# Kernel tuning notes

Hardware: AMD Instinct MI355X
Metric: run time of the kernel (lower is better)

The kernel has to match this reference:

```python
import jax, jax.numpy as jnp
import numpy as np

NUM_GRAPHS = 1024
NODES_PER_GRAPH = 128
AVG_DEG = 16
NODE_FEATS = 128
K = 20
TOTAL_LATENT = 97  # sum(latent_dim) = 32+32+32+1


def _init_params(key):
    def lin(k, fi, fo):
        s = 1.0 / np.sqrt(fi)
        kw, kb = jax.random.split(k)
        return (jax.random.uniform(kw, (fi, fo), jnp.float32, -s, s),
                jax.random.uniform(kb, (fo,), jnp.float32, -s, s))
    ks = jax.random.split(key, 9)
    p = {}
    p['W1'], p['b1'] = lin(ks[0], NODE_FEATS + 1, 32)
    p['W2'], p['b2'] = lin(ks[1], 32, 32)
    p['W3'], p['b3'] = lin(ks[2], 32, 32)
    p['W4'], p['b4'] = lin(ks[3], 32, 1)
    s = 1.0 / np.sqrt(TOTAL_LATENT)
    p['c1_w'] = jax.random.uniform(ks[4], (16, TOTAL_LATENT), jnp.float32, -s, s)
    p['c1_b'] = jnp.zeros((16,), jnp.float32)
    s2 = 1.0 / np.sqrt(16 * 5)
    p['c2_w'] = jax.random.uniform(ks[5], (32, 16, 5), jnp.float32, -s2, s2)
    p['c2_b'] = jnp.zeros((32,), jnp.float32)
    p['out_w'], p['out_b'] = lin(ks[6], 192, 1024)
    p['h1_w'], p['h1_b'] = lin(ks[7], 1024, 128)
    p['h2_w'], p['h2_b'] = lin(ks[8], 128, 16)
    return p


def setup_inputs() -> dict:
    key = jax.random.key(0)
    k_x, k_e, k_p = jax.random.split(key, 3)
    G, P, D = NUM_GRAPHS, NODES_PER_GRAPH, AVG_DEG
    N, E = G * P, G * P * D
    rng = np.random.default_rng(0)
    gid = np.repeat(np.arange(G, dtype=np.int64), P * D)
    src = gid * P + rng.integers(0, P, size=E)
    dst = gid * P + rng.integers(0, P, size=E)
    order = np.argsort(src, kind='stable')  # rows sorted by source node (matches slicing assumption)
    edge_index = jnp.asarray(np.stack([src[order], dst[order]]), dtype=jnp.int32)
    inp = {'x': jax.random.normal(k_x, (N, NODE_FEATS), jnp.float32),
           'edge_attr': jax.random.uniform(k_e, (E, 1), jnp.float32),
           'edge_index': edge_index}
    inp.update(_init_params(k_p))
    return inp


def reference(x, edge_attr, edge_index, W1, b1, W2, b2, W3, b3, W4, b4,
              c1_w, c1_b, c2_w, c2_b, out_w, out_b, h1_w, h1_b, h2_w, h2_b):
    N = x.shape[0]
    row, col = edge_index[0], edge_index[1]
    # per-source-node sum of incident edge attrs (replaces the Python slicing loop)
    x_edge = jax.ops.segment_sum(edge_attr, row, num_segments=N)  # [N,1]
    h = jnp.concatenate([x, x_edge], axis=1)  # [N, F+1]
    # GCN symmetric normalization with self-loops (PyG GCNConv default)
    deg = 1.0 + jax.ops.segment_sum(jnp.ones_like(col, dtype=jnp.float32), col, num_segments=N)
    dis = jax.lax.rsqrt(deg)
    enorm = dis[row] * dis[col]      # per-edge norm
    self_norm = dis * dis            # self-loop norm

    def gcn(h, W, b):
        h = h @ W
        agg = jax.ops.segment_sum(h[row] * enorm[:, None], col, num_segments=N)
        return agg + h * self_norm[:, None] + b

    o1 = gcn(h, W1, b1)
    o2 = gcn(o1, W2, b2)
    o3 = gcn(o2, W3, b3)
    o4 = gcn(o3, W4, b4)  # [N,1]
    feat = jnp.concatenate([o1, o2, o3, o4], axis=1)  # [N, 97]

    G = NUM_GRAPHS
    P = N // G
    scores = o4.reshape(G, P)
    _, idx = jax.lax.top_k(scores, K)  # per-graph top-k node indices (descending, sorted)
    pooled = jnp.take_along_axis(feat.reshape(G, P, TOTAL_LATENT), idx[:, :, None], axis=1)  # [G,K,97]

    # Conv1d(1,16,kernel=97,stride=97) over flattened [G,1,K*97] == per-slot matmul
    c1 = jax.nn.relu(jnp.einsum('gkd,cd->gck', pooled, c1_w) + c1_b[None, :, None])  # [G,16,K]
    mp = c1.reshape(G, 16, K // 2, 2).max(axis=-1)  # MaxPool1d(2,2) -> [G,16,10]
    c2 = jax.lax.conv_general_dilated(mp, c2_w, (1,), 'VALID',
                                      dimension_numbers=('NCH', 'OIH', 'NCH'))
    c2 = jax.nn.relu(c2 + c2_b[None, :, None])  # [G,32,6]
    dense = c2.reshape(G, -1)  # [G,192]
    d1 = jax.nn.relu(dense @ out_w + out_b)
    d2 = jax.nn.relu(d1 @ h1_w + h1_b)  # dropout is identity in eval mode
    logits = d2 @ h2_w + h2_b
    return jax.nn.log_softmax(logits, axis=1)
```

## Files before the change

### kernel.cpp

```cpp
#include <hip/hip_runtime.h>

typedef __attribute__((ext_vector_type(4))) float f4;
typedef __attribute__((ext_vector_type(2))) float f2;

#define NP 128
#define NE 2048
#define NFEAT 128
#define LW 33
#define NT 512

__device__ __forceinline__ void aggregate(float* zo, const float* __restrict__ bias,
    const unsigned char* inlist, const int* offs4, const int* indeg,
    const float* diss, int t)
{
  const int c = t >> 2;
  const int j0 = (t & 3) * 8;
  float s[8];
#pragma unroll
  for (int u = 0; u < 8; ++u) s[u] = zo[c*LW + j0 + u];
  const int ps = offs4[c];
  const int pe = ps + ((indeg[c] + 3) & ~3);
  for (int p = ps; p < pe; p += 4) {
    const unsigned w = *(const unsigned*)(inlist + p);
#pragma unroll
    for (int b = 0; b < 4; ++b) {
      const int rr = (w >> (8*b)) & 255;
#pragma unroll
      for (int u = 0; u < 8; ++u) s[u] += zo[rr*LW + j0 + u];
    }
  }
  __syncthreads();
  const float d = diss[c];
#pragma unroll
  for (int u = 0; u < 8; ++u) zo[c*LW + j0 + u] = d * s[u] + bias[j0 + u];
  __syncthreads();
}

__device__ __forceinline__ void mm32(const float* src, float* dst,
    const float* __restrict__ Wg, float* Wl, const float* diss, int t)
{
  if (t < 256) {
    const int k = t >> 3, jq = t & 7;
    *(f4*)&Wl[k*36 + jq*4] = *(const f4*)(Wg + (size_t)k*32 + jq*4);
  }
  __syncthreads();
  const int n2 = t & 63, c4 = t >> 6;
  float acc[2][4];
#pragma unroll
  for (int i = 0; i < 2; ++i)
#pragma unroll
    for (int u = 0; u < 4; ++u) acc[i][u] = 0.f;
#pragma unroll
  for (int k = 0; k < 32; ++k) {
    f4 w = *(const f4*)&Wl[k*36 + c4*4];
    const float a0 = src[n2*LW + k];
    const float a1 = src[(n2+64)*LW + k];
#pragma unroll
    for (int u = 0; u < 4; ++u) { acc[0][u] += a0 * w[u]; acc[1][u] += a1 * w[u]; }
  }
#pragma unroll
  for (int i = 0; i < 2; ++i) {
    const int n = n2 + 64*i;
    const float dd = diss[n];
#pragma unroll
    for (int u = 0; u < 4; ++u) dst[n*LW + c4*4 + u] = acc[i][u] * dd;
  }
}

__global__ __launch_bounds__(NT, 4) void k1_gcn(
    const float* __restrict__ x, const float* __restrict__ eattr,
    const int* __restrict__ eidx,
    const float* __restrict__ W1, const float* __restrict__ b1,
    const float* __restrict__ W2, const float* __restrict__ b2,
    const float* __restrict__ W3, const float* __restrict__ b3,
    const float* __restrict__ W4, const float* __restrict__ b4,
    const float* __restrict__ c1w, const float* __restrict__ c1b,
    const float* __restrict__ c2w, const float* __restrict__ c2b,
    float* __restrict__ dense_out, int E_total)
{
  __shared__ float o1[129*LW];
  __shared__ float o2[129*LW];
  __shared__ float o3[129*LW];
  __shared__ float Wl[32*36];
  __shared__ float o4s[129];
  __shared__ float xedge[NP];
  __shared__ float diss[NP];
  __shared__ int indeg[NP];
  __shared__ int offs4[NP];
  __shared__ int curp[NP];
  __shared__ unsigned char inlist[2432];

  const int t = threadIdx.x;
  const int g = blockIdx.x;
  const int ebase = g * NE;
  const int nbase = g * NP;

  if (t < NP) { xedge[t] = 0.f; indeg[t] = 0; curp[t] = 0; }
  for (int w = t; w < 608; w += NT) ((int*)inlist)[w] = (int)0x80808080u;
  __syncthreads();

  int er[4], ec[4];
#pragma unroll
  for (int i = 0; i < 4; ++i) {
    const int e = t + i * NT;
    er[i] = eidx[ebase + e] - nbase;
    ec[i] = eidx[E_total + ebase + e] - nbase;
    atomicAdd(&xedge[er[i]], eattr[ebase + e]);
    atomicAdd(&indeg[ec[i]], 1);
  }
  __syncthreads();

  if (t < NP) {
    int s = 0;
    for (int m = 0; m < NP; ++m) { const int dd = (indeg[m] + 3) & ~3; s += (m < t) ? dd : 0; }
    offs4[t] = s;
    diss[t] = rsqrtf(1.0f + (float)indeg[t]);
  }
  __syncthreads();

#pragma unroll
  for (int i = 0; i < 4; ++i) {
    const int p = atomicAdd(&curp[ec[i]], 1);
    inlist[offs4[ec[i]] + p] = (unsigned char)er[i];
  }

  {
    float* xs = o2;
    const int n2 = t & 63, c4 = t >> 6;
    const int sn = t >> 2, sq = t & 3;
    const float* xrow = x + (size_t)(nbase + sn) * NFEAT + sq * 8;
    f4 pv0 = *(const f4*)(xrow);
    f4 pv1 = *(const f4*)(xrow + 4);
    float acc[2][4];
#pragma unroll
    for (int i = 0; i < 2; ++i)
#pragma unroll
      for (int u = 0; u < 4; ++u) acc[i][u] = 0.f;

    for (int fc = 0; fc < NFEAT; fc += 32) {
      __syncthreads();
      {
        float* xd = xs + sn * LW + sq * 8;
#pragma unroll
        for (int j = 0; j < 4; ++j) xd[j] = pv0[j];
#pragma unroll
        for (int j = 0; j < 4; ++j) xd[4 + j] = pv1[j];
      }
      if (t < 256) {
        const int k = t >> 3, jq = t & 7;
        *(f4*)&Wl[k*36 + jq*4] = *(const f4*)(W1 + (size_t)(fc + k) * 32 + jq * 4);
      }
      if (fc < 96) {
        pv0 = *(const f4*)(xrow + fc + 32);
        pv1 = *(const f4*)(xrow + fc + 36);
      }
      __syncthreads();
#pragma unroll
      for (int k = 0; k < 32; ++k) {
        f4 w = *(const f4*)&Wl[k*36 + c4*4];
        const float a0 = xs[n2*LW + k];
        const float a1 = xs[(n2+64)*LW + k];
#pragma unroll
        for (int u = 0; u < 4; ++u) { acc[0][u] += a0 * w[u]; acc[1][u] += a1 * w[u]; }
      }
    }
    f4 wlast = *(const f4*)(W1 + 128*32 + c4*4);
#pragma unroll
    for (int i = 0; i < 2; ++i) {
      const int n = n2 + 64*i;
      const float xe = xedge[n], dd = diss[n];
#pragma unroll
      for (int u = 0; u < 4; ++u)
        o1[n*LW + c4*4 + u] = (acc[i][u] + xe * wlast[u]) * dd;
    }
  }
  __syncthreads();
  if (t < LW) { o1[128*LW + t] = 0.f; o2[128*LW + t] = 0.f; o3[128*LW + t] = 0.f; }
  if (t == 0) o4s[128] = 0.f;
  __syncthreads();

  aggregate(o1, b1, inlist, offs4, indeg, diss, t);
  mm32(o1, o2, W2, Wl, diss, t);
  __syncthreads();
  aggregate(o2, b2, inlist, offs4, indeg, diss, t);
  mm32(o2, o3, W3, Wl, diss, t);
  __syncthreads();
  aggregate(o3, b3, inlist, offs4, indeg, diss, t);

  if (t < NP) {
    float s = 0.f;
#pragma unroll
    for (int f = 0; f < 32; ++f) s += o3[t*LW + f] * W4[f];
    o4s[t] = s * diss[t];
  }
  __syncthreads();
  float s4 = 0.f;
  if (t < NP) {
    s4 = o4s[t];
    const int ps = offs4[t], pe = ps + ((indeg[t] + 3) & ~3);
    for (int p = ps; p < pe; p += 4) {
      const unsigned w = *(const unsigned*)(inlist + p);
#pragma unroll
      for (int b = 0; b < 4; ++b) s4 += o4s[(w >> (8*b)) & 255];
    }
  }
  __syncthreads();
  if (t < NP) o4s[t] = diss[t] * s4 + b4[0];
  __syncthreads();

  int* selidx   = (int*)Wl;
  float* c1buf  = Wl + 32;
  float* mpbuf  = Wl + 352;
  if (t < NP) {
    const float sn = o4s[t];
    int cnt = 0;
    for (int m = 0; m < NP; ++m) {
      const float sm = o4s[m];
      cnt += (sm > sn || (sm == sn && m < t)) ? 1 : 0;
    }
    if (cnt < 20) selidx[cnt] = t;
  }
  __syncthreads();

  if (t < 320) {
    const int k = t % 20, ch = t / 20;
    const int nd = selidx[k];
    const float* wr = c1w + ch * 97;
    float s = c1b[ch];
#pragma unroll 8
    for (int d = 0; d < 32; ++d) s += o1[nd*LW + d] * wr[d];
#pragma unroll 8
    for (int d = 0; d < 32; ++d) s += o2[nd*LW + d] * wr[32 + d];
#pragma unroll 8
    for (int d = 0; d < 32; ++d) s += o3[nd*LW + d] * wr[64 + d];
    s += o4s[nd] * wr[96];
    c1buf[ch*20 + k] = fmaxf(s, 0.f);
  }
  __syncthreads();
  if (t < 160) {
    const int ch = t / 10, p = t % 10;
    mpbuf[ch*10 + p] = fmaxf(c1buf[ch*20 + 2*p], c1buf[ch*20 + 2*p + 1]);
  }
  __syncthreads();
  if (t < 192) {
    const int oc = t / 6, tt = t % 6;
    float s = c2b[oc];
#pragma unroll
    for (int ic = 0; ic < 16; ++ic) {
      const float* wr = c2w + (oc * 16 + ic) * 5;
#pragma unroll
      for (int u = 0; u < 5; ++u) s += mpbuf[ic*10 + tt + u] * wr[u];
    }
    dense_out[(size_t)g * 192 + t] = fmaxf(s, 0.f);
  }
}

__global__ __launch_bounds__(256) void k2_d1(const float* __restrict__ dense,
    const float* __restrict__ out_w, const float* __restrict__ out_b,
    float* __restrict__ d1)
{
  __shared__ float As[32 * 68];
  __shared__ float Bs[32 * 68];
  const int t = threadIdx.x;
  const int n0 = blockIdx.x * 64, m0 = blockIdx.y * 64;
  const int r = t & 15, c = t >> 4;
  float acc[4][4];
#pragma unroll
  for (int i = 0; i < 4; ++i)
#pragma unroll
    for (int u = 0; u < 4; ++u) acc[i][u] = 0.f;

  for (int kk = 0; kk < 192; kk += 32) {
    __syncthreads();
    {
      const int m = t >> 2;
      const int kq = (t & 3) * 2;
#pragma unroll
      for (int q = 0; q < 2; ++q) {
        f4 v = *(const f4*)(dense + (size_t)(m0 + m) * 192 + kk + (kq + q) * 4);
        const int k0 = (kq + q) * 4;
        As[(k0+0)*68 + m] = v[0]; As[(k0+1)*68 + m] = v[1];
        As[(k0+2)*68 + m] = v[2]; As[(k0+3)*68 + m] = v[3];
      }
    }
    {
      const int k = t >> 3;
      const int nq = (t & 7) * 2;
#pragma unroll
      for (int q = 0; q < 2; ++q) {
        f4 v = *(const f4*)(out_w + (size_t)(kk + k) * 1024 + n0 + (nq + q) * 4);
        *(f4*)&Bs[k*68 + (nq + q) * 4] = v;
      }
    }
    __syncthreads();
#pragma unroll
    for (int k = 0; k < 32; ++k) {
      f4 a = *(const f4*)&As[k*68 + r*4];
      f4 b = *(const f4*)&Bs[k*68 + c*4];
#pragma unroll
      for (int i = 0; i < 4; ++i)
#pragma unroll
        for (int u = 0; u < 4; ++u) acc[i][u] += a[i] * b[u];
    }
  }
  f4 bb = *(const f4*)(out_b + n0 + c*4);
#pragma unroll
  for (int i = 0; i < 4; ++i) {
    f4 o;
#pragma unroll
    for (int u = 0; u < 4; ++u) o[u] = fmaxf(acc[i][u] + bb[u], 0.f);
    *(f4*)(d1 + (size_t)(m0 + r*4 + i) * 1024 + n0 + c*4) = o;
  }
}

__global__ __launch_bounds__(256) void k3_init(const float* __restrict__ h1_b,
    float* __restrict__ d2)
{
  const int i = blockIdx.x * 256 + threadIdx.x;
  d2[i] = h1_b[i & 127];
}

__global__ __launch_bounds__(256) void k3_d2(const float* __restrict__ d1,
    const float* __restrict__ h1_w, float* __restrict__ d2)
{
  __shared__ float As[32 * 36];
  __shared__ float Bs[32 * 36];
  const int t = threadIdx.x;
  const int m0 = blockIdx.x * 32, n0 = blockIdx.y * 32, ks = blockIdx.z * 128;
  const int r = t & 15, c = t >> 4;
  float a00 = 0.f, a01 = 0.f, a10 = 0.f, a11 = 0.f;

  for (int kk = ks; kk < ks + 128; kk += 32) {
    __syncthreads();
    {
      const int m = t >> 3, kq = t & 7;
      f4 v = *(const f4*)(d1 + (size_t)(m0 + m) * 1024 + kk + kq * 4);
      const int k0 = kq * 4;
      As[(k0+0)*36 + m] = v[0]; As[(k0+1)*36 + m] = v[1];
      As[(k0+2)*36 + m] = v[2]; As[(k0+3)*36 + m] = v[3];
    }
    {
      const int k = t >> 3, nq = t & 7;
      f4 v = *(const f4*)(h1_w + (size_t)(kk + k) * 128 + n0 + nq * 4);
      *(f4*)&Bs[k*36 + nq*4] = v;
    }
    __syncthreads();
#pragma unroll
    for (int k = 0; k < 32; ++k) {
      f2 a = *(const f2*)&As[k*36 + r*2];
      f2 b = *(const f2*)&Bs[k*36 + c*2];
      a00 += a[0]*b[0]; a01 += a[0]*b[1];
      a10 += a[1]*b[0]; a11 += a[1]*b[1];
    }
  }
  atomicAdd(d2 + (size_t)(m0 + r*2 + 0) * 128 + n0 + c*2 + 0, a00);
  atomicAdd(d2 + (size_t)(m0 + r*2 + 0) * 128 + n0 + c*2 + 1, a01);
  atomicAdd(d2 + (size_t)(m0 + r*2 + 1) * 128 + n0 + c*2 + 0, a10);
  atomicAdd(d2 + (size_t)(m0 + r*2 + 1) * 128 + n0 + c*2 + 1, a11);
}

__global__ __launch_bounds__(256) void k4_out(const float* __restrict__ d2,
    const float* __restrict__ h2_w, const float* __restrict__ h2_b,
    float* __restrict__ outp)
{
  __shared__ float lbuf[16][17];
  const int t = threadIdx.x;
  const int gl = t >> 4, cc = t & 15;
  const int g = blockIdx.x * 16 + gl;
  float s = h2_b[cc];
  for (int k4 = 0; k4 < 32; ++k4) {
    f4 v = *(const f4*)(d2 + (size_t)g * 128 + k4 * 4);
#pragma unroll
    for (int i = 0; i < 4; ++i) {
      const float rv = fmaxf(v[i], 0.f);
      s += rv * h2_w[(k4*4 + i) * 16 + cc];
    }
  }
  lbuf[gl][cc] = s;
  __syncthreads();
  float mx = -1e30f;
#pragma unroll
  for (int j = 0; j < 16; ++j) mx = fmaxf(mx, lbuf[gl][j]);
  float se = 0.f;
#pragma unroll
  for (int j = 0; j < 16; ++j) se += expf(lbuf[gl][j] - mx);
  outp[(size_t)g * 16 + cc] = s - mx - logf(se);
}

extern "C" void kernel_launch(void* const* d_in, const int* in_sizes, int n_in,
                              void* d_out, int out_size, void* d_ws, size_t ws_size,
                              hipStream_t stream) {
  const float* x     = (const float*)d_in[0];
  const float* eattr = (const float*)d_in[1];
  const int*   eidx  = (const int*)d_in[2];
  const float* W1 = (const float*)d_in[3];  const float* b1 = (const float*)d_in[4];
  const float* W2 = (const float*)d_in[5];  const float* b2 = (const float*)d_in[6];
  const float* W3 = (const float*)d_in[7];  const float* b3 = (const float*)d_in[8];
  const float* W4 = (const float*)d_in[9];  const float* b4 = (const float*)d_in[10];
  const float* c1w = (const float*)d_in[11]; const float* c1b = (const float*)d_in[12];
  const float* c2w = (const float*)d_in[13]; const float* c2b = (const float*)d_in[14];
  const float* out_w = (const float*)d_in[15]; const float* out_b = (const float*)d_in[16];
  const float* h1_w  = (const float*)d_in[17]; const float* h1_b  = (const float*)d_in[18];
  const float* h2_w  = (const float*)d_in[19]; const float* h2_b  = (const float*)d_in[20];

  const int E_total = in_sizes[1];
  const int N_nodes = in_sizes[0] / NFEAT;
  const int G = N_nodes / NP;

  float* ws    = (float*)d_ws;
  float* dense = ws;
  float* d1    = ws + (size_t)G * 192;
  float* d2    = d1 + (size_t)G * 1024;

  k1_gcn<<<G, NT, 0, stream>>>(x, eattr, eidx, W1, b1, W2, b2, W3, b3, W4, b4,
                               c1w, c1b, c2w, c2b, dense, E_total);
  k2_d1<<<dim3(16, G / 64), 256, 0, stream>>>(dense, out_w, out_b, d1);
  k3_init<<<(G * 128) / 256, 256, 0, stream>>>(h1_b, d2);
  k3_d2<<<dim3(G / 32, 4, 8), 256, 0, stream>>>(d1, h1_w, d2);
  k4_out<<<G / 16, 256, 0, stream>>>(d2, h2_w, h2_b, (float*)d_out);
}
```

Measured before the change: 141.9 us.

## Pad rows to 36 floats, vectorize aggregation, read weights from global

Changes the per-node LDS row stride from 33 to 36 so that aggregation and matmuls can use float4 loads and stores. Aggregation now walks an unpadded byte adjacency list one neighbor at a time instead of in padded groups of four, which removes the sentinel row and the list initialization. The matmuls are remapped so each wavefront owns an 8-column slice of 64 nodes and reads weights from global memory with wave-uniform addresses, dropping the LDS weight staging and its barrier. The first-layer input is double-buffered across o2/o3, and the k3 inner loop switches from float2 to scalar LDS reads. The risk is more LDS bank conflicts with the stride-36 layout and extra global/scalar weight traffic.

```diff
diff --git a/kernel.cpp b/kernel.cpp
--- a/kernel.cpp
+++ b/kernel.cpp
@@ -1,70 +1,60 @@
 #include <hip/hip_runtime.h>
 
 typedef __attribute__((ext_vector_type(4))) float f4;
-typedef __attribute__((ext_vector_type(2))) float f2;
 
 #define NP 128
 #define NE 2048
 #define NFEAT 128
-#define LW 33
+#define LW 36
 #define NT 512
 
 __device__ __forceinline__ void aggregate(float* zo, const float* __restrict__ bias,
-    const unsigned char* inlist, const int* offs4, const int* indeg,
+    const unsigned char* inlist, const int* offs, const int* indeg,
     const float* diss, int t)
 {
   const int c = t >> 2;
   const int j0 = (t & 3) * 8;
-  float s[8];
-#pragma unroll
-  for (int u = 0; u < 8; ++u) s[u] = zo[c*LW + j0 + u];
-  const int ps = offs4[c];
-  const int pe = ps + ((indeg[c] + 3) & ~3);
-  for (int p = ps; p < pe; p += 4) {
-    const unsigned w = *(const unsigned*)(inlist + p);
-#pragma unroll
-    for (int b = 0; b < 4; ++b) {
-      const int rr = (w >> (8*b)) & 255;
-#pragma unroll
-      for (int u = 0; u < 8; ++u) s[u] += zo[rr*LW + j0 + u];
-    }
+  float* zr = zo + c * LW + j0;
+  f4 s0 = *(const f4*)zr;
+  f4 s1 = *(const f4*)(zr + 4);
+  const int ps = offs[c], pe = ps + indeg[c];
+  for (int p = ps; p < pe; ++p) {
+    const int rr = inlist[p];
+    const float* nr = zo + rr * LW + j0;
+    s0 += *(const f4*)nr;
+    s1 += *(const f4*)(nr + 4);
   }
   __syncthreads();
   const float d = diss[c];
-#pragma unroll
-  for (int u = 0; u < 8; ++u) zo[c*LW + j0 + u] = d * s[u] + bias[j0 + u];
+  const f4 b0 = *(const f4*)(bias + j0);
+  const f4 b1 = *(const f4*)(bias + j0 + 4);
+  *(f4*)zr = s0 * d + b0;
+  *(f4*)(zr + 4) = s1 * d + b1;
   __syncthreads();
 }
 
 __device__ __forceinline__ void mm32(const float* src, float* dst,
-    const float* __restrict__ Wg, float* Wl, const float* diss, int t)
-{
-  if (t < 256) {
-    const int k = t >> 3, jq = t & 7;
-    *(f4*)&Wl[k*36 + jq*4] = *(const f4*)(Wg + (size_t)k*32 + jq*4);
-  }
-  __syncthreads();
-  const int n2 = t & 63, c4 = t >> 6;
-  float acc[2][4];
-#pragma unroll
-  for (int i = 0; i < 2; ++i)
-#pragma unroll
-    for (int u = 0; u < 4; ++u) acc[i][u] = 0.f;
+    const float* __restrict__ Wg, const float* diss, int t)
+{
+  const int wv = __builtin_amdgcn_readfirstlane(t >> 6);
+  const int j0 = (wv & 3) * 8;
+  const int c  = ((wv >> 2) * 64) + (t & 63);
+  f4 av[8];
+#pragma unroll
+  for (int j = 0; j < 8; ++j) av[j] = *(const f4*)(src + c * LW + 4 * j);
+  f4 a0 = {0.f, 0.f, 0.f, 0.f}, a1 = {0.f, 0.f, 0.f, 0.f};
 #pragma unroll
   for (int k = 0; k < 32; ++k) {
-    f4 w = *(const f4*)&Wl[k*36 + c4*4];
-    const float a0 = src[n2*LW + k];
-    const float a1 = src[(n2+64)*LW + k];
-#pragma unroll
-    for (int u = 0; u < 4; ++u) { acc[0][u] += a0 * w[u]; acc[1][u] += a1 * w[u]; }
-  }
-#pragma unroll
-  for (int i = 0; i < 2; ++i) {
-    const int n = n2 + 64*i;
-    const float dd = diss[n];
-#pragma unroll
-    for (int u = 0; u < 4; ++u) dst[n*LW + c4*4 + u] = acc[i][u] * dd;
-  }
+    const float a = av[k >> 2][k & 3];
+    const float* wr = Wg + k * 32 + j0;
+    const f4 w0 = *(const f4*)wr;
+    const f4 w1 = *(const f4*)(wr + 4);
+    a0 += a * w0;
+    a1 += a * w1;
+  }
+  const float d = diss[c];
+  *(f4*)(dst + c * LW + j0) = a0 * d;
+  *(f4*)(dst + c * LW + j0 + 4) = a1 * d;
 }
 
 __global__ __launch_bounds__(NT, 4) void k1_gcn(
@@ -78,17 +68,19 @@
     const float* __restrict__ c2w, const float* __restrict__ c2b,
     float* __restrict__ dense_out, int E_total)
 {
-  __shared__ float o1[129*LW];
-  __shared__ float o2[129*LW];
-  __shared__ float o3[129*LW];
-  __shared__ float Wl[32*36];
-  __shared__ float o4s[129];
+  __shared__ float o1[NP * LW];
+  __shared__ float o2[NP * LW];
+  __shared__ float o3[NP * LW];
+  __shared__ float o4s[NP];
   __shared__ float xedge[NP];
   __shared__ float diss[NP];
   __shared__ int indeg[NP];
-  __shared__ int offs4[NP];
+  __shared__ int offs[NP];
   __shared__ int curp[NP];
-  __shared__ unsigned char inlist[2432];
+  __shared__ unsigned char inlist[NE];
+  __shared__ int selidx[20];
+  __shared__ float c1buf[16 * 20];
+  __shared__ float mpbuf[16 * 10];
 
   const int t = threadIdx.x;
   const int g = blockIdx.x;
@@ -96,7 +88,6 @@
   const int nbase = g * NP;
 
   if (t < NP) { xedge[t] = 0.f; indeg[t] = 0; curp[t] = 0; }
-  for (int w = t; w < 608; w += NT) ((int*)inlist)[w] = (int)0x80808080u;
   __syncthreads();
 
   int er[4], ec[4];
@@ -112,8 +103,8 @@
 
   if (t < NP) {
     int s = 0;
-    for (int m = 0; m < NP; ++m) { const int dd = (indeg[m] + 3) & ~3; s += (m < t) ? dd : 0; }
-    offs4[t] = s;
+    for (int m = 0; m < NP; ++m) s += (m < t) ? indeg[m] : 0;
+    offs[t] = s;
     diss[t] = rsqrtf(1.0f + (float)indeg[t]);
   }
   __syncthreads();
@@ -121,96 +112,77 @@
 #pragma unroll
   for (int i = 0; i < 4; ++i) {
     const int p = atomicAdd(&curp[ec[i]], 1);
-    inlist[offs4[ec[i]] + p] = (unsigned char)er[i];
+    inlist[offs[ec[i]] + p] = (unsigned char)er[i];
   }
 
   {
-    float* xs = o2;
-    const int n2 = t & 63, c4 = t >> 6;
+    const int wv = __builtin_amdgcn_readfirstlane(t >> 6);
+    const int j0 = (wv & 3) * 8;
+    const int c  = ((wv >> 2) * 64) + (t & 63);
     const int sn = t >> 2, sq = t & 3;
     const float* xrow = x + (size_t)(nbase + sn) * NFEAT + sq * 8;
     f4 pv0 = *(const f4*)(xrow);
     f4 pv1 = *(const f4*)(xrow + 4);
-    float acc[2][4];
-#pragma unroll
-    for (int i = 0; i < 2; ++i)
-#pragma unroll
-      for (int u = 0; u < 4; ++u) acc[i][u] = 0.f;
+    f4 a0 = {0.f, 0.f, 0.f, 0.f}, a1 = {0.f, 0.f, 0.f, 0.f};
 
     for (int fc = 0; fc < NFEAT; fc += 32) {
+      float* xs = (fc & 32) ? o3 : o2;
       __syncthreads();
-      {
-        float* xd = xs + sn * LW + sq * 8;
-#pragma unroll
-        for (int j = 0; j < 4; ++j) xd[j] = pv0[j];
-#pragma unroll
-        for (int j = 0; j < 4; ++j) xd[4 + j] = pv1[j];
-      }
-      if (t < 256) {
-        const int k = t >> 3, jq = t & 7;
-        *(f4*)&Wl[k*36 + jq*4] = *(const f4*)(W1 + (size_t)(fc + k) * 32 + jq * 4);
-      }
+      *(f4*)(xs + sn * LW + sq * 8) = pv0;
+      *(f4*)(xs + sn * LW + sq * 8 + 4) = pv1;
       if (fc < 96) {
         pv0 = *(const f4*)(xrow + fc + 32);
         pv1 = *(const f4*)(xrow + fc + 36);
       }
       __syncthreads();
+      f4 av[8];
+#pragma unroll
+      for (int j = 0; j < 8; ++j) av[j] = *(const f4*)(xs + c * LW + 4 * j);
+      const float* Wc = W1 + (size_t)fc * 32;
 #pragma unroll
       for (int k = 0; k < 32; ++k) {
-        f4 w = *(const f4*)&Wl[k*36 + c4*4];
-        const float a0 = xs[n2*LW + k];
-        const float a1 = xs[(n2+64)*LW + k];
-#pragma unroll
-        for (int u = 0; u < 4; ++u) { acc[0][u] += a0 * w[u]; acc[1][u] += a1 * w[u]; }
+        const float a = av[k >> 2][k & 3];
+        const float* wr = Wc + k * 32 + j0;
+        const f4 w0 = *(const f4*)wr;
+        const f4 w1 = *(const f4*)(wr + 4);
+        a0 += a * w0;
+        a1 += a * w1;
       }
     }
-    f4 wlast = *(const f4*)(W1 + 128*32 + c4*4);
-#pragma unroll
-    for (int i = 0; i < 2; ++i) {
-      const int n = n2 + 64*i;
-      const float xe = xedge[n], dd = diss[n];
-#pragma unroll
-      for (int u = 0; u < 4; ++u)
-        o1[n*LW + c4*4 + u] = (acc[i][u] + xe * wlast[u]) * dd;
-    }
-  }
-  __syncthreads();
-  if (t < LW) { o1[128*LW + t] = 0.f; o2[128*LW + t] = 0.f; o3[128*LW + t] = 0.f; }
-  if (t == 0) o4s[128] = 0.f;
-  __syncthreads();
-
-  aggregate(o1, b1, inlist, offs4, indeg, diss, t);
-  mm32(o1, o2, W2, Wl, diss, t);
-  __syncthreads();
-  aggregate(o2, b2, inlist, offs4, indeg, diss, t);
-  mm32(o2, o3, W3, Wl, diss, t);
-  __syncthreads();
-  aggregate(o3, b3, inlist, offs4, indeg, diss, t);
+    const float xe = xedge[c];
+    const float d = diss[c];
+    const f4 wl0 = *(const f4*)(W1 + 128 * 32 + j0);
+    const f4 wl1 = *(const f4*)(W1 + 128 * 32 + j0 + 4);
+    *(f4*)(o1 + c * LW + j0) = (a0 + xe * wl0) * d;
+    *(f4*)(o1 + c * LW + j0 + 4) = (a1 + xe * wl1) * d;
+  }
+  __syncthreads();
+
+  aggregate(o1, b1, inlist, offs, indeg, diss, t);
+  mm32(o1, o2, W2, diss, t);
+  __syncthreads();
+  aggregate(o2, b2, inlist, offs, indeg, diss, t);
+  mm32(o2, o3, W3, diss, t);
+  __syncthreads();
+  aggregate(o3, b3, inlist, offs, indeg, diss, t);
 
   if (t < NP) {
     float s = 0.f;
 #pragma unroll
-    for (int f = 0; f < 32; ++f) s += o3[t*LW + f] * W4[f];
+    for (int f = 0; f < 32; ++f) s += o3[t * LW + f] * W4[f];
     o4s[t] = s * diss[t];
   }
   __syncthreads();
   float s4 = 0.f;
   if (t < NP) {
     s4 = o4s[t];
-    const int ps = offs4[t], pe = ps + ((indeg[t] + 3) & ~3);
-    for (int p = ps; p < pe; p += 4) {
-      const unsigned w = *(const unsigned*)(inlist + p);
-#pragma unroll
-      for (int b = 0; b < 4; ++b) s4 += o4s[(w >> (8*b)) & 255];
-    }
+    const int ps = offs[t], pe = ps + indeg[t];
+    for (int p = ps; p < pe; ++p) s4 += o4s[inlist[p]];
   }
   __syncthreads();
   if (t < NP) o4s[t] = diss[t] * s4 + b4[0];
   __syncthreads();
 
-  int* selidx   = (int*)Wl;
-  float* c1buf  = Wl + 32;
-  float* mpbuf  = Wl + 352;
   if (t < NP) {
     const float sn = o4s[t];
     int cnt = 0;
@@ -228,18 +200,18 @@
     const float* wr = c1w + ch * 97;
     float s = c1b[ch];
 #pragma unroll 8
-    for (int d = 0; d < 32; ++d) s += o1[nd*LW + d] * wr[d];
+    for (int d = 0; d < 32; ++d) s += o1[nd * LW + d] * wr[d];
 #pragma unroll 8
-    for (int d = 0; d < 32; ++d) s += o2[nd*LW + d] * wr[32 + d];
+    for (int d = 0; d < 32; ++d) s += o2[nd * LW + d] * wr[32 + d];
 #pragma unroll 8
-    for (int d = 0; d < 32; ++d) s += o3[nd*LW + d] * wr[64 + d];
+    for (int d = 0; d < 32; ++d) s += o3[nd * LW + d] * wr[64 + d];
     s += o4s[nd] * wr[96];
-    c1buf[ch*20 + k] = fmaxf(s, 0.f);
+    c1buf[ch * 20 + k] = fmaxf(s, 0.f);
   }
   __syncthreads();
   if (t < 160) {
     const int ch = t / 10, p = t % 10;
-    mpbuf[ch*10 + p] = fmaxf(c1buf[ch*20 + 2*p], c1buf[ch*20 + 2*p + 1]);
+    mpbuf[ch * 10 + p] = fmaxf(c1buf[ch * 20 + 2 * p], c1buf[ch * 20 + 2 * p + 1]);
   }
   __syncthreads();
   if (t < 192) {
@@ -249,7 +221,7 @@
     for (int ic = 0; ic < 16; ++ic) {
       const float* wr = c2w + (oc * 16 + ic) * 5;
 #pragma unroll
-      for (int u = 0; u < 5; ++u) s += mpbuf[ic*10 + tt + u] * wr[u];
+      for (int u = 0; u < 5; ++u) s += mpbuf[ic * 10 + tt + u] * wr[u];
     }
     dense_out[(size_t)g * 192 + t] = fmaxf(s, 0.f);
   }
@@ -347,10 +319,10 @@
     __syncthreads();
 #pragma unroll
     for (int k = 0; k < 32; ++k) {
-      f2 a = *(const f2*)&As[k*36 + r*2];
-      f2 b = *(const f2*)&Bs[k*36 + c*2];
-      a00 += a[0]*b[0]; a01 += a[0]*b[1];
-      a10 += a[1]*b[0]; a11 += a[1]*b[1];
+      const float a0 = As[k*36 + r*2], a1 = As[k*36 + r*2 + 1];
+      const float b0 = Bs[k*36 + c*2], b1 = Bs[k*36 + c*2 + 1];
+      a00 += a0*b0; a01 += a0*b1;
+      a10 += a1*b0; a11 += a1*b1;
     }
   }
   atomicAdd(d2 + (size_t)(m0 + r*2 + 0) * 128 + n0 + c*2 + 0, a00);
```

Measured after the change: 158.1 us. 11.4% more time.

## Cut GCN kernel LDS to two ping-pong buffers, spill o1 to global, degree-sort aggregation

Applied to the files above, without the earlier changes.

The fused GCN kernel now keeps two 129x33 shared buffers instead of three, swapping roles between layers. The first-layer output is written to a global workspace and gathered back only for the top-k rows needed by the conv stage. Aggregation threads are assigned nodes in descending in-degree order to balance work across wavefronts, and the x tile prefetch is hoisted to the kernel start. The aim is lower LDS use per block, allowing more resident blocks, at the cost of extra global writes and reads plus a rank sort.

```diff
diff --git a/kernel.cpp b/kernel.cpp
--- a/kernel.cpp
+++ b/kernel.cpp
@@ -11,28 +11,42 @@
 
 __device__ __forceinline__ void aggregate(float* zo, const float* __restrict__ bias,
     const unsigned char* inlist, const int* offs4, const int* indeg,
-    const float* diss, int t)
-{
-  const int c = t >> 2;
+    const float* diss, const int* order, int t, float* __restrict__ gout)
+{
+  const int n = order[t >> 2];
   const int j0 = (t & 3) * 8;
   float s[8];
 #pragma unroll
-  for (int u = 0; u < 8; ++u) s[u] = zo[c*LW + j0 + u];
-  const int ps = offs4[c];
-  const int pe = ps + ((indeg[c] + 3) & ~3);
+  for (int u = 0; u < 4; ++u) {
+    f2 v = *(const f2*)&zo[n*LW + j0 + 2*u];
+    s[2*u] = v[0]; s[2*u+1] = v[1];
+  }
+  const int ps = offs4[n];
+  const int pe = ps + ((indeg[n] + 3) & ~3);
   for (int p = ps; p < pe; p += 4) {
     const unsigned w = *(const unsigned*)(inlist + p);
 #pragma unroll
     for (int b = 0; b < 4; ++b) {
       const int rr = (w >> (8*b)) & 255;
 #pragma unroll
-      for (int u = 0; u < 8; ++u) s[u] += zo[rr*LW + j0 + u];
-    }
-  }
-  __syncthreads();
-  const float d = diss[c];
-#pragma unroll
-  for (int u = 0; u < 8; ++u) zo[c*LW + j0 + u] = d * s[u] + bias[j0 + u];
+      for (int u = 0; u < 4; ++u) {
+        f2 v = *(const f2*)&zo[rr*LW + j0 + 2*u];
+        s[2*u] += v[0]; s[2*u+1] += v[1];
+      }
+    }
+  }
+  __syncthreads();
+  const float d = diss[n];
+#pragma unroll
+  for (int u = 0; u < 8; ++u) s[u] = d * s[u] + bias[j0 + u];
+#pragma unroll
+  for (int u = 0; u < 8; ++u) zo[n*LW + j0 + u] = s[u];
+  if (gout) {
+    f4 v0 = {s[0], s[1], s[2], s[3]};
+    f4 v1 = {s[4], s[5], s[6], s[7]};
+    *(f4*)(gout + n*32 + j0) = v0;
+    *(f4*)(gout + n*32 + j0 + 4) = v1;
+  }
   __syncthreads();
 }
 
@@ -45,26 +59,22 @@
   }
   __syncthreads();
   const int n2 = t & 63, c4 = t >> 6;
-  float acc[2][4];
-#pragma unroll
-  for (int i = 0; i < 2; ++i)
-#pragma unroll
-    for (int u = 0; u < 4; ++u) acc[i][u] = 0.f;
+  f4 a0 = {0.f,0.f,0.f,0.f}, a1 = {0.f,0.f,0.f,0.f};
 #pragma unroll
   for (int k = 0; k < 32; ++k) {
-    f4 w = *(const f4*)&Wl[k*36 + c4*4];
-    const float a0 = src[n2*LW + k];
-    const float a1 = src[(n2+64)*LW + k];
-#pragma unroll
-    for (int u = 0; u < 4; ++u) { acc[0][u] += a0 * w[u]; acc[1][u] += a1 * w[u]; }
-  }
-#pragma unroll
-  for (int i = 0; i < 2; ++i) {
-    const int n = n2 + 64*i;
-    const float dd = diss[n];
-#pragma unroll
-    for (int u = 0; u < 4; ++u) dst[n*LW + c4*4 + u] = acc[i][u] * dd;
-  }
+    const f4 w = *(const f4*)&Wl[k*36 + c4*4];
+    const float x0 = src[n2*LW + k];
+    const float x1 = src[(n2+64)*LW + k];
+    a0 += x0 * w;
+    a1 += x1 * w;
+  }
+  const float d0 = diss[n2], d1 = diss[n2 + 64];
+#pragma unroll
+  for (int u = 0; u < 4; ++u) {
+    dst[n2*LW + c4*4 + u] = a0[u] * d0;
+    dst[(n2+64)*LW + c4*4 + u] = a1[u] * d1;
+  }
+  __syncthreads();
 }
 
 __global__ __launch_bounds__(NT, 4) void k1_gcn(
@@ -76,11 +86,10 @@
     const float* __restrict__ W4, const float* __restrict__ b4,
     const float* __restrict__ c1w, const float* __restrict__ c1b,
     const float* __restrict__ c2w, const float* __restrict__ c2b,
-    float* __restrict__ dense_out, int E_total)
-{
-  __shared__ float o1[129*LW];
-  __shared__ float o2[129*LW];
-  __shared__ float o3[129*LW];
+    float* __restrict__ o1g_all, float* __restrict__ dense_out, int E_total)
+{
+  __shared__ float A[129*LW];
+  __shared__ float B[129*LW];
   __shared__ float Wl[32*36];
   __shared__ float o4s[129];
   __shared__ float xedge[NP];
@@ -88,14 +97,23 @@
   __shared__ int indeg[NP];
   __shared__ int offs4[NP];
   __shared__ int curp[NP];
+  __shared__ int order[NP];
   __shared__ unsigned char inlist[2432];
 
   const int t = threadIdx.x;
   const int g = blockIdx.x;
   const int ebase = g * NE;
   const int nbase = g * NP;
+  float* __restrict__ o1g = o1g_all + (size_t)g * (NP * 32);
+
+  const int sn = t >> 2, sq = t & 3;
+  const float* xrow = x + (size_t)(nbase + sn) * NFEAT + sq * 8;
+  f4 pv0 = *(const f4*)(xrow);
+  f4 pv1 = *(const f4*)(xrow + 4);
 
   if (t < NP) { xedge[t] = 0.f; indeg[t] = 0; curp[t] = 0; }
+  if (t < LW) { A[128*LW + t] = 0.f; B[128*LW + t] = 0.f; }
+  if (t == 0) o4s[128] = 0.f;
   for (int w = t; w < 608; w += NT) ((int*)inlist)[w] = (int)0x80808080u;
   __syncthreads();
 
@@ -112,9 +130,16 @@
 
   if (t < NP) {
     int s = 0;
-    for (int m = 0; m < NP; ++m) { const int dd = (indeg[m] + 3) & ~3; s += (m < t) ? dd : 0; }
+    for (int m = 0; m < NP; ++m) s += (m < t) ? ((indeg[m] + 3) & ~3) : 0;
     offs4[t] = s;
     diss[t] = rsqrtf(1.0f + (float)indeg[t]);
+    const int dn = indeg[t];
+    int r = 0;
+    for (int m = 0; m < NP; ++m) {
+      const int dm = indeg[m];
+      r += (dm > dn || (dm == dn && m < t)) ? 1 : 0;
+    }
+    order[r] = t;
   }
   __syncthreads();
 
@@ -125,27 +150,13 @@
   }
 
   {
-    float* xs = o2;
     const int n2 = t & 63, c4 = t >> 6;
-    const int sn = t >> 2, sq = t & 3;
-    const float* xrow = x + (size_t)(nbase + sn) * NFEAT + sq * 8;
-    f4 pv0 = *(const f4*)(xrow);
-    f4 pv1 = *(const f4*)(xrow + 4);
-    float acc[2][4];
-#pragma unroll
-    for (int i = 0; i < 2; ++i)
-#pragma unroll
-      for (int u = 0; u < 4; ++u) acc[i][u] = 0.f;
-
+    f4 a0 = {0.f,0.f,0.f,0.f}, a1 = {0.f,0.f,0.f,0.f};
     for (int fc = 0; fc < NFEAT; fc += 32) {
+      float* xs = (fc & 32) ? B : A;
       __syncthreads();
-      {
-        float* xd = xs + sn * LW + sq * 8;
-#pragma unroll
-        for (int j = 0; j < 4; ++j) xd[j] = pv0[j];
-#pragma unroll
-        for (int j = 0; j < 4; ++j) xd[4 + j] = pv1[j];
-      }
+      *(f4*)(xs + sn * LW + sq * 8) = pv0;
+      *(f4*)(xs + sn * LW + sq * 8 + 4) = pv1;
       if (t < 256) {
         const int k = t >> 3, jq = t & 7;
         *(f4*)&Wl[k*36 + jq*4] = *(const f4*)(W1 + (size_t)(fc + k) * 32 + jq * 4);
@@ -157,40 +168,37 @@
       __syncthreads();
 #pragma unroll
       for (int k = 0; k < 32; ++k) {
-        f4 w = *(const f4*)&Wl[k*36 + c4*4];
-        const float a0 = xs[n2*LW + k];
-        const float a1 = xs[(n2+64)*LW + k];
-#pragma unroll
-        for (int u = 0; u < 4; ++u) { acc[0][u] += a0 * w[u]; acc[1][u] += a1 * w[u]; }
-      }
-    }
-    f4 wlast = *(const f4*)(W1 + 128*32 + c4*4);
-#pragma unroll
-    for (int i = 0; i < 2; ++i) {
-      const int n = n2 + 64*i;
-      const float xe = xedge[n], dd = diss[n];
-#pragma unroll
-      for (int u = 0; u < 4; ++u)
-        o1[n*LW + c4*4 + u] = (acc[i][u] + xe * wlast[u]) * dd;
-    }
-  }
-  __syncthreads();
-  if (t < LW) { o1[128*LW + t] = 0.f; o2[128*LW + t] = 0.f; o3[128*LW + t] = 0.f; }
-  if (t == 0) o4s[128] = 0.f;
-  __syncthreads();
-
-  aggregate(o1, b1, inlist, offs4, indeg, diss, t);
-  mm32(o1, o2, W2, Wl, diss, t);
-  __syncthreads();
-  aggregate(o2, b2, inlist, offs4, indeg, diss, t);
-  mm32(o2, o3, W3, Wl, diss, t);
-  __syncthreads();
-  aggregate(o3, b3, inlist, offs4, indeg, diss, t);
+        const f4 w = *(const f4*)&Wl[k*36 + c4*4];
+        const float x0 = xs[n2*LW + k];
+        const float x1 = xs[(n2+64)*LW + k];
+        a0 += x0 * w;
+        a1 += x1 * w;
+      }
+    }
+    const f4 wl = *(const f4*)(W1 + 128*32 + c4*4);
+    const float xe0 = xedge[n2], d0 = diss[n2];
+    const float xe1 = xedge[n2+64], d1 = diss[n2+64];
+    a0 = (a0 + xe0 * wl) * d0;
+    a1 = (a1 + xe1 * wl) * d1;
+    __syncthreads();
+#pragma unroll
+    for (int u = 0; u < 4; ++u) {
+      A[n2*LW + c4*4 + u] = a0[u];
+      A[(n2+64)*LW + c4*4 + u] = a1[u];
+    }
+  }
+  __syncthreads();
+
+  aggregate(A, b1, inlist, offs4, indeg, diss, order, t, o1g);
+  mm32(A, B, W2, Wl, diss, t);
+  aggregate(B, b2, inlist, offs4, indeg, diss, order, t, nullptr);
+  mm32(B, A, W3, Wl, diss, t);
+  aggregate(A, b3, inlist, offs4, indeg, diss, order, t, nullptr);
 
   if (t < NP) {
     float s = 0.f;
 #pragma unroll
-    for (int f = 0; f < 32; ++f) s += o3[t*LW + f] * W4[f];
+    for (int f = 0; f < 32; ++f) s += A[t*LW + f] * W4[f];
     o4s[t] = s * diss[t];
   }
   __syncthreads();
@@ -208,17 +216,24 @@
   if (t < NP) o4s[t] = diss[t] * s4 + b4[0];
   __syncthreads();
 
-  int* selidx   = (int*)Wl;
-  float* c1buf  = Wl + 32;
-  float* mpbuf  = Wl + 352;
+  int* selidx   = curp;
+  float* c1buf  = Wl;
+  float* mpbuf  = Wl + 320;
+  float* s1stg  = Wl + 480;
   if (t < NP) {
-    const float sn = o4s[t];
+    const float sn_ = o4s[t];
     int cnt = 0;
     for (int m = 0; m < NP; ++m) {
       const float sm = o4s[m];
-      cnt += (sm > sn || (sm == sn && m < t)) ? 1 : 0;
+      cnt += (sm > sn_ || (sm == sn_ && m < t)) ? 1 : 0;
     }
     if (cnt < 20) selidx[cnt] = t;
+  }
+  __syncthreads();
+
+  for (int w = t; w < 640; w += NT) {
+    const int kk = w >> 5, col = w & 31;
+    s1stg[kk * LW + col] = o1g[selidx[kk] * 32 + col];
   }
   __syncthreads();
 
@@ -228,18 +243,18 @@
     const float* wr = c1w + ch * 97;
     float s = c1b[ch];
 #pragma unroll 8
-    for (int d = 0; d < 32; ++d) s += o1[nd*LW + d] * wr[d];
+    for (int d = 0; d < 32; ++d) s += s1stg[k*LW + d] * wr[d];
 #pragma unroll 8
-    for (int d = 0; d < 32; ++d) s += o2[nd*LW + d] * wr[32 + d];
+    for (int d = 0; d < 32; ++d) s += B[nd*LW + d] * wr[32 + d];
 #pragma unroll 8
-    for (int d = 0; d < 32; ++d) s += o3[nd*LW + d] * wr[64 + d];
+    for (int d = 0; d < 32; ++d) s += A[nd*LW + d] * wr[64 + d];
     s += o4s[nd] * wr[96];
-    c1buf[ch*20 + k] = fmaxf(s, 0.f);
+    c1buf[ch * 20 + k] = fmaxf(s, 0.f);
   }
   __syncthreads();
   if (t < 160) {
     const int ch = t / 10, p = t % 10;
-    mpbuf[ch*10 + p] = fmaxf(c1buf[ch*20 + 2*p], c1buf[ch*20 + 2*p + 1]);
+    mpbuf[ch * 10 + p] = fmaxf(c1buf[ch * 20 + 2*p], c1buf[ch * 20 + 2*p + 1]);
   }
   __syncthreads();
   if (t < 192) {
@@ -249,7 +264,7 @@
     for (int ic = 0; ic < 16; ++ic) {
       const float* wr = c2w + (oc * 16 + ic) * 5;
 #pragma unroll
-      for (int u = 0; u < 5; ++u) s += mpbuf[ic*10 + tt + u] * wr[u];
+      for (int u = 0; u < 5; ++u) s += mpbuf[ic * 10 + tt + u] * wr[u];
     }
     dense_out[(size_t)g * 192 + t] = fmaxf(s, 0.f);
   }
@@ -276,9 +291,9 @@
       const int m = t >> 2;
       const int kq = (t & 3) * 2;
 #pragma unroll
-      for (int q = 0; q < 2; ++q) {
-        f4 v = *(const f4*)(dense + (size_t)(m0 + m) * 192 + kk + (kq + q) * 4);
-        const int k0 = (kq + q) * 4;
+      for (int qq = 0; qq < 2; ++qq) {
+        f4 v = *(const f4*)(dense + (size_t)(m0 + m) * 192 + kk + (kq + qq) * 4);
+        const int k0 = (kq + qq) * 4;
         As[(k0+0)*68 + m] = v[0]; As[(k0+1)*68 + m] = v[1];
         As[(k0+2)*68 + m] = v[2]; As[(k0+3)*68 + m] = v[3];
       }
@@ -287,9 +302,9 @@
       const int k = t >> 3;
       const int nq = (t & 7) * 2;
 #pragma unroll
-      for (int q = 0; q < 2; ++q) {
-        f4 v = *(const f4*)(out_w + (size_t)(kk + k) * 1024 + n0 + (nq + q) * 4);
-        *(f4*)&Bs[k*68 + (nq + q) * 4] = v;
+      for (int qq = 0; qq < 2; ++qq) {
+        f4 v = *(const f4*)(out_w + (size_t)(kk + k) * 1024 + n0 + (nq + qq) * 4);
+        *(f4*)&Bs[k*68 + (nq + qq) * 4] = v;
       }
     }
     __syncthreads();
@@ -347,10 +362,10 @@
     __syncthreads();
 #pragma unroll
     for (int k = 0; k < 32; ++k) {
-      f2 a = *(const f2*)&As[k*36 + r*2];
-      f2 b = *(const f2*)&Bs[k*36 + c*2];
-      a00 += a[0]*b[0]; a01 += a[0]*b[1];
-      a10 += a[1]*b[0]; a11 += a[1]*b[1];
+      const float a0 = As[k*36 + r*2], a1 = As[k*36 + r*2 + 1];
+      const float b0 = Bs[k*36 + c*2], b1 = Bs[k*36 + c*2 + 1];
+      a00 += a0*b0; a01 += a0*b1;
+      a10 += a1*b0; a11 += a1*b1;
     }
   }
   atomicAdd(d2 + (size_t)(m0 + r*2 + 0) * 128 + n0 + c*2 + 0, a00);
@@ -411,9 +426,10 @@
   float* dense = ws;
   float* d1    = ws + (size_t)G * 192;
   float* d2    = d1 + (size_t)G * 1024;
+  float* o1g   = d2 + (size_t)G * 128;
 
   k1_gcn<<<G, NT, 0, stream>>>(x, eattr, eidx, W1, b1, W2, b2, W3, b3, W4, b4,
-                               c1w, c1b, c2w, c2b, dense, E_total);
+                               c1w, c1b, c2w, c2b, o1g, dense, E_total);
   k2_d1<<<dim3(16, G / 64), 256, 0, stream>>>(dense, out_w, out_b, d1);
   k3_init<<<(G * 128) / 256, 256, 0, stream>>>(h1_b, d2);
   k3_d2<<<dim3(G / 32, 4, 8), 256, 0, stream>>>(d1, h1_w, d2);
```

Result: slower. 286.9 us (+102.1%).

## Ping-pong two LDS buffers, spill layer-1 output to global, dual-accumulator aggregation

Applied to the files above, without the earlier changes.

The GCN kernel now keeps only two shared activation buffers instead of three and alternates between them across layers. The first layer's output goes to a global scratch buffer, and the 20 selected rows are gathered back from it for the conv stage. The aggregation loop now processes edges 8 at a time into two independent accumulator sets, with adjacency lists padded to multiples of 8. The aim is to cut LDS use so more blocks fit per CU and to add ILP in the gather, at the cost of extra global traffic and more padding work.

```diff
diff --git a/kernel.cpp b/kernel.cpp
--- a/kernel.cpp
+++ b/kernel.cpp
@@ -10,29 +10,50 @@
 #define NT 512
 
 __device__ __forceinline__ void aggregate(float* zo, const float* __restrict__ bias,
-    const unsigned char* inlist, const int* offs4, const int* indeg,
-    const float* diss, int t)
+    const unsigned char* inlist, const int* offs, const int* indeg,
+    const float* diss, int t, float* __restrict__ gout)
 {
   const int c = t >> 2;
   const int j0 = (t & 3) * 8;
+  float sa[8], sb[8];
+#pragma unroll
+  for (int u = 0; u < 4; ++u) {
+    f2 v = *(const f2*)&zo[c*LW + j0 + 2*u];
+    sa[2*u] = v[0]; sa[2*u+1] = v[1];
+    sb[2*u] = 0.f;  sb[2*u+1] = 0.f;
+  }
+  const int ps = offs[c];
+  const int ne8 = (indeg[c] + 7) & ~7;
+  const unsigned* il = (const unsigned*)(inlist + ps);
+  for (int p = 0; p < ne8; p += 8) {
+    const unsigned w0 = il[(p >> 2)];
+    const unsigned w1 = il[(p >> 2) + 1];
+#pragma unroll
+    for (int b = 0; b < 4; ++b) {
+      const int r0 = (w0 >> (8*b)) & 255;
+      const int r1 = (w1 >> (8*b)) & 255;
+#pragma unroll
+      for (int u = 0; u < 4; ++u) {
+        f2 v0 = *(const f2*)&zo[r0*LW + j0 + 2*u];
+        f2 v1 = *(const f2*)&zo[r1*LW + j0 + 2*u];
+        sa[2*u] += v0[0]; sa[2*u+1] += v0[1];
+        sb[2*u] += v1[0]; sb[2*u+1] += v1[1];
+      }
+    }
+  }
+  __syncthreads();
+  const float d = diss[c];
   float s[8];
 #pragma unroll
-  for (int u = 0; u < 8; ++u) s[u] = zo[c*LW + j0 + u];
-  const int ps = offs4[c];
-  const int pe = ps + ((indeg[c] + 3) & ~3);
-  for (int p = ps; p < pe; p += 4) {
-    const unsigned w = *(const unsigned*)(inlist + p);
-#pragma unroll
-    for (int b = 0; b < 4; ++b) {
-      const int rr = (w >> (8*b)) & 255;
-#pragma unroll
-      for (int u = 0; u < 8; ++u) s[u] += zo[rr*LW + j0 + u];
-    }
-  }
-  __syncthreads();
-  const float d = diss[c];
-#pragma unroll
-  for (int u = 0; u < 8; ++u) zo[c*LW + j0 + u] = d * s[u] + bias[j0 + u];
+  for (int u = 0; u < 8; ++u) s[u] = d * (sa[u] + sb[u]) + bias[j0 + u];
+#pragma unroll
+  for (int u = 0; u < 8; ++u) zo[c*LW + j0 + u] = s[u];
+  if (gout) {
+    f4 v0 = {s[0], s[1], s[2], s[3]};
+    f4 v1 = {s[4], s[5], s[6], s[7]};
+    *(f4*)(gout + c*32 + j0) = v0;
+    *(f4*)(gout + c*32 + j0 + 4) = v1;
+  }
   __syncthreads();
 }
 
@@ -76,27 +97,29 @@
     const float* __restrict__ W4, const float* __restrict__ b4,
     const float* __restrict__ c1w, const float* __restrict__ c1b,
     const float* __restrict__ c2w, const float* __restrict__ c2b,
-    float* __restrict__ dense_out, int E_total)
-{
-  __shared__ float o1[129*LW];
-  __shared__ float o2[129*LW];
-  __shared__ float o3[129*LW];
+    float* __restrict__ o1g_all, float* __restrict__ dense_out, int E_total)
+{
+  __shared__ float A[129*LW];
+  __shared__ float B[129*LW];
   __shared__ float Wl[32*36];
   __shared__ float o4s[129];
   __shared__ float xedge[NP];
   __shared__ float diss[NP];
   __shared__ int indeg[NP];
-  __shared__ int offs4[NP];
+  __shared__ int offs[NP];
   __shared__ int curp[NP];
-  __shared__ unsigned char inlist[2432];
+  __shared__ unsigned char inlist[2944];
 
   const int t = threadIdx.x;
   const int g = blockIdx.x;
   const int ebase = g * NE;
   const int nbase = g * NP;
+  float* __restrict__ o1g = o1g_all + (size_t)g * (NP * 32);
 
   if (t < NP) { xedge[t] = 0.f; indeg[t] = 0; curp[t] = 0; }
-  for (int w = t; w < 608; w += NT) ((int*)inlist)[w] = (int)0x80808080u;
+  if (t < LW) { A[128*LW + t] = 0.f; B[128*LW + t] = 0.f; }
+  if (t == 0) o4s[128] = 0.f;
+  for (int w = t; w < 736; w += NT) ((int*)inlist)[w] = (int)0x80808080u;
   __syncthreads();
 
   int er[4], ec[4];
@@ -112,8 +135,8 @@
 
   if (t < NP) {
     int s = 0;
-    for (int m = 0; m < NP; ++m) { const int dd = (indeg[m] + 3) & ~3; s += (m < t) ? dd : 0; }
-    offs4[t] = s;
+    for (int m = 0; m < NP; ++m) s += (m < t) ? ((indeg[m] + 7) & ~7) : 0;
+    offs[t] = s;
     diss[t] = rsqrtf(1.0f + (float)indeg[t]);
   }
   __syncthreads();
@@ -121,11 +144,11 @@
 #pragma unroll
   for (int i = 0; i < 4; ++i) {
     const int p = atomicAdd(&curp[ec[i]], 1);
-    inlist[offs4[ec[i]] + p] = (unsigned char)er[i];
+    inlist[offs[ec[i]] + p] = (unsigned char)er[i];
   }
 
   {
-    float* xs = o2;
+    float* xs = B;
     const int n2 = t & 63, c4 = t >> 6;
     const int sn = t >> 2, sq = t & 3;
     const float* xrow = x + (size_t)(nbase + sn) * NFEAT + sq * 8;
@@ -165,41 +188,41 @@
       }
     }
     f4 wlast = *(const f4*)(W1 + 128*32 + c4*4);
+    __syncthreads();
 #pragma unroll
     for (int i = 0; i < 2; ++i) {
       const int n = n2 + 64*i;
       const float xe = xedge[n], dd = diss[n];
 #pragma unroll
       for (int u = 0; u < 4; ++u)
-        o1[n*LW + c4*4 + u] = (acc[i][u] + xe * wlast[u]) * dd;
-    }
-  }
-  __syncthreads();
-  if (t < LW) { o1[128*LW + t] = 0.f; o2[128*LW + t] = 0.f; o3[128*LW + t] = 0.f; }
-  if (t == 0) o4s[128] = 0.f;
-  __syncthreads();
-
-  aggregate(o1, b1, inlist, offs4, indeg, diss, t);
-  mm32(o1, o2, W2, Wl, diss, t);
-  __syncthreads();
-  aggregate(o2, b2, inlist, offs4, indeg, diss, t);
-  mm32(o2, o3, W3, Wl, diss, t);
-  __syncthreads();
-  aggregate(o3, b3, inlist, offs4, indeg, diss, t);
+        A[n*LW + c4*4 + u] = (acc[i][u] + xe * wlast[u]) * dd;
+    }
+  }
+  __syncthreads();
+
+  aggregate(A, b1, inlist, offs, indeg, diss, t, o1g);
+  mm32(A, B, W2, Wl, diss, t);
+  __syncthreads();
+  aggregate(B, b2, inlist, offs, indeg, diss, t, nullptr);
+  mm32(B, A, W3, Wl, diss, t);
+  __syncthreads();
+  aggregate(A, b3, inlist, offs, indeg, diss, t, nullptr);
 
   if (t < NP) {
     float s = 0.f;
 #pragma unroll
-    for (int f = 0; f < 32; ++f) s += o3[t*LW + f] * W4[f];
+    for (int f = 0; f < 32; ++f) s += A[t*LW + f] * W4[f];
     o4s[t] = s * diss[t];
   }
   __syncthreads();
   float s4 = 0.f;
   if (t < NP) {
     s4 = o4s[t];
-    const int ps = offs4[t], pe = ps + ((indeg[t] + 3) & ~3);
-    for (int p = ps; p < pe; p += 4) {
-      const unsigned w = *(const unsigned*)(inlist + p);
+    const int ps = offs[t];
+    const int ne8 = (indeg[t] + 7) & ~7;
+    const unsigned* il = (const unsigned*)(inlist + ps);
+    for (int p = 0; p < ne8; p += 4) {
+      const unsigned w = il[p >> 2];
 #pragma unroll
       for (int b = 0; b < 4; ++b) s4 += o4s[(w >> (8*b)) & 255];
     }
@@ -208,17 +231,24 @@
   if (t < NP) o4s[t] = diss[t] * s4 + b4[0];
   __syncthreads();
 
-  int* selidx   = (int*)Wl;
-  float* c1buf  = Wl + 32;
-  float* mpbuf  = Wl + 352;
+  int* selidx  = curp;
+  float* c1buf = Wl;
+  float* mpbuf = Wl + 320;
+  float* s1stg = Wl + 480;
   if (t < NP) {
-    const float sn = o4s[t];
+    const float sn_ = o4s[t];
     int cnt = 0;
     for (int m = 0; m < NP; ++m) {
       const float sm = o4s[m];
-      cnt += (sm > sn || (sm == sn && m < t)) ? 1 : 0;
+      cnt += (sm > sn_ || (sm == sn_ && m < t)) ? 1 : 0;
     }
     if (cnt < 20) selidx[cnt] = t;
+  }
+  __syncthreads();
+
+  for (int w = t; w < 640; w += NT) {
+    const int kk = w >> 5, col = w & 31;
+    s1stg[kk * LW + col] = o1g[selidx[kk] * 32 + col];
   }
   __syncthreads();
 
@@ -228,18 +258,18 @@
     const float* wr = c1w + ch * 97;
     float s = c1b[ch];
 #pragma unroll 8
-    for (int d = 0; d < 32; ++d) s += o1[nd*LW + d] * wr[d];
+    for (int d = 0; d < 32; ++d) s += s1stg[k*LW + d] * wr[d];
 #pragma unroll 8
-    for (int d = 0; d < 32; ++d) s += o2[nd*LW + d] * wr[32 + d];
+    for (int d = 0; d < 32; ++d) s += B[nd*LW + d] * wr[32 + d];
 #pragma unroll 8
-    for (int d = 0; d < 32; ++d) s += o3[nd*LW + d] * wr[64 + d];
+    for (int d = 0; d < 32; ++d) s += A[nd*LW + d] * wr[64 + d];
     s += o4s[nd] * wr[96];
-    c1buf[ch*20 + k] = fmaxf(s, 0.f);
+    c1buf[ch * 20 + k] = fmaxf(s, 0.f);
   }
   __syncthreads();
   if (t < 160) {
     const int ch = t / 10, p = t % 10;
-    mpbuf[ch*10 + p] = fmaxf(c1buf[ch*20 + 2*p], c1buf[ch*20 + 2*p + 1]);
+    mpbuf[ch * 10 + p] = fmaxf(c1buf[ch * 20 + 2*p], c1buf[ch * 20 + 2*p + 1]);
   }
   __syncthreads();
   if (t < 192) {
@@ -249,7 +279,7 @@
     for (int ic = 0; ic < 16; ++ic) {
       const float* wr = c2w + (oc * 16 + ic) * 5;
 #pragma unroll
-      for (int u = 0; u < 5; ++u) s += mpbuf[ic*10 + tt + u] * wr[u];
+      for (int u = 0; u < 5; ++u) s += mpbuf[ic * 10 + tt + u] * wr[u];
     }
     dense_out[(size_t)g * 192 + t] = fmaxf(s, 0.f);
   }
@@ -276,9 +306,9 @@
       const int m = t >> 2;
       const int kq = (t & 3) * 2;
 #pragma unroll
-      for (int q = 0; q < 2; ++q) {
-        f4 v = *(const f4*)(dense + (size_t)(m0 + m) * 192 + kk + (kq + q) * 4);
-        const int k0 = (kq + q) * 4;
+      for (int qq = 0; qq < 2; ++qq) {
+        f4 v = *(const f4*)(dense + (size_t)(m0 + m) * 192 + kk + (kq + qq) * 4);
+        const int k0 = (kq + qq) * 4;
         As[(k0+0)*68 + m] = v[0]; As[(k0+1)*68 + m] = v[1];
         As[(k0+2)*68 + m] = v[2]; As[(k0+3)*68 + m] = v[3];
       }
@@ -287,9 +317,9 @@
       const int k = t >> 3;
       const int nq = (t & 7) * 2;
 #pragma unroll
-      for (int q = 0; q < 2; ++q) {
-        f4 v = *(const f4*)(out_w + (size_t)(kk + k) * 1024 + n0 + (nq + q) * 4);
-        *(f4*)&Bs[k*68 + (nq + q) * 4] = v;
+      for (int qq = 0; qq < 2; ++qq) {
+        f4 v = *(const f4*)(out_w + (size_t)(kk + k) * 1024 + n0 + (nq + qq) * 4);
+        *(f4*)&Bs[k*68 + (nq + qq) * 4] = v;
       }
     }
     __syncthreads();
@@ -347,10 +377,10 @@
     __syncthreads();
 #pragma unroll
     for (int k = 0; k < 32; ++k) {
-      f2 a = *(const f2*)&As[k*36 + r*2];
-      f2 b = *(const f2*)&Bs[k*36 + c*2];
-      a00 += a[0]*b[0]; a01 += a[0]*b[1];
-      a10 += a[1]*b[0]; a11 += a[1]*b[1];
+      const float a0 = As[k*36 + r*2], a1 = As[k*36 + r*2 + 1];
+      const float b0 = Bs[k*36 + c*2], b1 = Bs[k*36 + c*2 + 1];
+      a00 += a0*b0; a01 += a0*b1;
+      a10 += a1*b0; a11 += a1*b1;
     }
   }
   atomicAdd(d2 + (size_t)(m0 + r*2 + 0) * 128 + n0 + c*2 + 0, a00);
@@ -411,9 +441,10 @@
   float* dense = ws;
   float* d1    = ws + (size_t)G * 192;
   float* d2    = d1 + (size_t)G * 1024;
+  float* o1g   = d2 + (size_t)G * 128;
 
   k1_gcn<<<G, NT, 0, stream>>>(x, eattr, eidx, W1, b1, W2, b2, W3, b3, W4, b4,
-                               c1w, c1b, c2w, c2b, dense, E_total);
+                               c1w, c1b, c2w, c2b, o1g, dense, E_total);
   k2_d1<<<dim3(16, G / 64), 256, 0, stream>>>(dense, out_w, out_b, d1);
   k3_init<<<(G * 128) / 256, 256, 0, stream>>>(h1_b, d2);
   k3_d2<<<dim3(G / 32, 4, 8), 256, 0, stream>>>(d1, h1_w, d2);
```

New measurement: 292.8 us. +106.3%, slower.
